# Kernel optimization log

Hardware: AMD Instinct MI355X
Metric: run time of the kernel (lower is better)

The kernel has to match this reference:

```python
import math
import jax, jax.numpy as jnp
import numpy as np

B, L, D, H, DFF = 2, 2048, 1024, 16, 4096
HD = D // H
NUM_BUCKETS, MAX_DISTANCE = 32, 128


def setup_inputs() -> dict:
    key = jax.random.key(0)
    ks = jax.random.split(key, 10)
    s = 0.02
    return {
        "hidden_states": jax.random.normal(ks[0], (B, L, D), dtype=jnp.float32),
        "Wq": jax.random.normal(ks[1], (D, D), dtype=jnp.float32) * s,
        "Wk": jax.random.normal(ks[2], (D, D), dtype=jnp.float32) * s,
        "Wv": jax.random.normal(ks[3], (D, D), dtype=jnp.float32) * s,
        "Wo": jax.random.normal(ks[4], (D, D), dtype=jnp.float32) * s,
        "W1": jax.random.normal(ks[5], (D, DFF), dtype=jnp.float32) * s,
        "W2": jax.random.normal(ks[6], (DFF, D), dtype=jnp.float32) * s,
        "ln1_g": jnp.ones((D,), dtype=jnp.float32),
        "ln2_g": jnp.ones((D,), dtype=jnp.float32),
        "rel_table": jax.random.normal(ks[7], (NUM_BUCKETS, H), dtype=jnp.float32) * s,
    }


def rms_norm(x, g, eps=1e-6):
    # T5-style LayerNorm: scale only, no mean subtraction
    var = jnp.mean(jnp.square(x.astype(jnp.float32)), axis=-1, keepdims=True)
    return (x.astype(jnp.float32) * jax.lax.rsqrt(var + eps)).astype(x.dtype) * g


def relative_position_bias(seq_len, table):
    # bidirectional T5 bucket scheme, num_buckets=32, max_distance=128
    ctx = jnp.arange(seq_len)[:, None]
    mem = jnp.arange(seq_len)[None, :]
    rp = mem - ctx                                  # (L, L) int
    nb = NUM_BUCKETS // 2
    buckets = (rp > 0).astype(jnp.int32) * nb
    rpa = jnp.abs(rp)
    max_exact = nb // 2
    is_small = rpa < max_exact
    safe = jnp.maximum(rpa, 1).astype(jnp.float32)  # avoid log(0); masked by is_small
    large = max_exact + (
        jnp.log(safe / max_exact) / math.log(MAX_DISTANCE / max_exact) * (nb - max_exact)
    ).astype(jnp.int32)
    large = jnp.minimum(large, nb - 1)
    buckets = buckets + jnp.where(is_small, rpa, large)   # (L, L)
    vals = table[buckets]                                  # (L, L, H)
    return jnp.transpose(vals, (2, 0, 1))[None]            # (1, H, L, L)


def reference(hidden_states, Wq, Wk, Wv, Wo, W1, W2, ln1_g, ln2_g, rel_table):
    x = hidden_states
    b, l, d = x.shape

    # --- self-attention sublayer (pre-norm) ---
    h = rms_norm(x, ln1_g)
    q = (h @ Wq).reshape(b, l, H, HD)
    k = (h @ Wk).reshape(b, l, H, HD)
    v = (h @ Wv).reshape(b, l, H, HD)

    bias = relative_position_bias(l, rel_table)            # (1, H, L, L)
    # NOTE: source's manual attention path has NO 1/sqrt(head_dim) scaling
    scores = jnp.einsum("bqhd,bkhd->bhqk", q, k) + bias
    attn = jax.nn.softmax(scores.astype(jnp.float32), axis=-1).astype(scores.dtype)
    out = jnp.einsum("bhqk,bkhd->bqhd", attn, v).reshape(b, l, d)
    x = x + out @ Wo

    # --- feed-forward sublayer (pre-norm) ---
    h = rms_norm(x, ln2_g)
    x = x + jax.nn.relu(h @ W1) @ W2
    return x
```

## Files before the change

kernel.cpp:

```cpp
#include <hip/hip_runtime.h>
#include <hip/hip_bf16.h>
#include <math.h>

#define BDIM 1024
#define HEADS 16
#define HDIM 64
#define LSEQ 2048
#define NBATCH 2
#define DFFDIM 4096
#define QKVN 3072
#define LOG2E 1.44269504f

typedef __bf16 bf16x8_t __attribute__((ext_vector_type(8)));
typedef float f32x4_t __attribute__((ext_vector_type(4)));

__device__ __forceinline__ ushort f2bf(float f) {
    union { __hip_bfloat16 b; ushort u; } cv;
    cv.b = __float2bfloat16(f);
    return cv.u;
}
__device__ __forceinline__ float bf2f(ushort u) {
    union { unsigned int i; float f; } cv;
    cv.i = ((unsigned int)u) << 16;
    return cv.f;
}

__global__ __launch_bounds__(256) void transpose_cvt(const float* __restrict__ W,
                                                     ushort* __restrict__ Wt,
                                                     int K, int N) {
    __shared__ ushort tile[32][33];
    int bi = blockIdx.y;
    int bj = blockIdx.x;
    int tx = threadIdx.x;
    int ty = threadIdx.y;
#pragma unroll
    for (int r = 0; r < 4; ++r) {
        int krow = bi * 32 + ty + r * 8;
        int ncol = bj * 32 + tx;
        tile[ty + r * 8][tx] = f2bf(W[(size_t)krow * N + ncol]);
    }
    __syncthreads();
#pragma unroll
    for (int r = 0; r < 4; ++r) {
        int nrow = bj * 32 + ty + r * 8;
        int kcol = bi * 32 + tx;
        Wt[(size_t)nrow * K + kcol] = tile[tx][ty + r * 8];
    }
}

__global__ __launch_bounds__(256) void vtrans(const ushort* __restrict__ qkv,
                                              ushort* __restrict__ vT) {
    __shared__ ushort t[64][72];
    const int ktile = blockIdx.x;
    const int bh = blockIdx.y;
    const int b = bh >> 4, h = bh & 15;
    const int tid = threadIdx.x;
    const int r = tid >> 2;
    const int c0 = (tid & 3) * 16;
    const ushort* src = qkv + (size_t)(b * LSEQ + ktile * 64 + r) * QKVN + 2048 + h * HDIM + c0;
    union { bf16x8_t v; ushort s[8]; } u0, u1;
    u0.v = *(const bf16x8_t*)src;
    u1.v = *(const bf16x8_t*)(src + 8);
#pragma unroll
    for (int j = 0; j < 8; ++j) { t[r][c0 + j] = u0.s[j]; t[r][c0 + 8 + j] = u1.s[j]; }
    __syncthreads();
    const int hd = tid >> 2;
    union { bf16x8_t v; ushort s[8]; } w0, w1;
#pragma unroll
    for (int j = 0; j < 8; ++j) { w0.s[j] = t[c0 + j][hd]; w1.s[j] = t[c0 + 8 + j][hd]; }
    ushort* dst = vT + (size_t)(bh * HDIM + hd) * LSEQ + ktile * 64 + c0;
    *(bf16x8_t*)dst = w0.v;
    *(bf16x8_t*)(dst + 8) = w1.v;
}

__global__ __launch_bounds__(256) void rmsnorm_k(const float* __restrict__ x,
                                                 const float* __restrict__ g,
                                                 ushort* __restrict__ out) {
    int row = blockIdx.x;
    int t = threadIdx.x;
    int w = t >> 6, l = t & 63;
    const float4 v = reinterpret_cast<const float4*>(x + (size_t)row * BDIM)[t];
    float ss = v.x * v.x + v.y * v.y + v.z * v.z + v.w * v.w;
#pragma unroll
    for (int m = 1; m <= 32; m <<= 1) ss += __shfl_xor(ss, m);
    __shared__ float wsum[4];
    if (l == 0) wsum[w] = ss;
    __syncthreads();
    float tot = wsum[0] + wsum[1] + wsum[2] + wsum[3];
    float r = rsqrtf(tot * (1.0f / BDIM) + 1e-6f);
    const float4 gv = reinterpret_cast<const float4*>(g)[t];
    ushort4 o;
    o.x = f2bf(v.x * r * gv.x);
    o.y = f2bf(v.y * r * gv.y);
    o.z = f2bf(v.z * r * gv.z);
    o.w = f2bf(v.w * r * gv.w);
    reinterpret_cast<ushort4*>(out + (size_t)row * BDIM)[t] = o;
}

__global__ void bias_table_k(const float* __restrict__ rel, float* __restrict__ btab) {
    int idx = blockIdx.x * 256 + threadIdx.x;
    if (idx >= HEADS * 4095) return;
    int h = idx / 4095;
    int d = idx % 4095;
    int rp = d - 2047;
    int bucket = rp > 0 ? 16 : 0;
    int rpa = rp < 0 ? -rp : rp;
    if (rpa < 8) {
        bucket += rpa;
    } else {
        int large = 8 + (int)(logf((float)rpa * 0.125f) * (1.0f / logf(16.0f)) * 8.0f);
        bucket += large < 15 ? large : 15;
    }
    btab[idx] = rel[bucket * HEADS + h];
}

__global__ __launch_bounds__(256) void reduce2_k(const ushort* __restrict__ parts,
                                                 const float* __restrict__ res,
                                                 float* __restrict__ out,
                                                 size_t mn) {
    size_t i = ((size_t)blockIdx.x * 256 + threadIdx.x) * 4;
    float4 r = *(const float4*)(res + i);
    ushort4 a = *(const ushort4*)(parts + i);
    ushort4 b = *(const ushort4*)(parts + mn + i);
    float4 o;
    o.x = r.x + bf2f(a.x) + bf2f(b.x);
    o.y = r.y + bf2f(a.y) + bf2f(b.y);
    o.z = r.z + bf2f(a.z) + bf2f(b.z);
    o.w = r.w + bf2f(a.w) + bf2f(b.w);
    *(float4*)(out + i) = o;
}

__global__ __launch_bounds__(256) void reduce2_rms(const ushort* __restrict__ parts,
                                                   const float* __restrict__ res,
                                                   const float* __restrict__ g,
                                                   float* __restrict__ out,
                                                   ushort* __restrict__ hout,
                                                   size_t mn) {
    int row = blockIdx.x;
    int t = threadIdx.x;
    int w = t >> 6, l = t & 63;
    size_t i = (size_t)row * BDIM + t * 4;
    float4 r = *(const float4*)(res + i);
    ushort4 a = *(const ushort4*)(parts + i);
    ushort4 b = *(const ushort4*)(parts + mn + i);
    float4 o;
    o.x = r.x + bf2f(a.x) + bf2f(b.x);
    o.y = r.y + bf2f(a.y) + bf2f(b.y);
    o.z = r.z + bf2f(a.z) + bf2f(b.z);
    o.w = r.w + bf2f(a.w) + bf2f(b.w);
    *(float4*)(out + i) = o;
    float ss = o.x * o.x + o.y * o.y + o.z * o.z + o.w * o.w;
#pragma unroll
    for (int m = 1; m <= 32; m <<= 1) ss += __shfl_xor(ss, m);
    __shared__ float wsum[4];
    if (l == 0) wsum[w] = ss;
    __syncthreads();
    float tot = wsum[0] + wsum[1] + wsum[2] + wsum[3];
    float rr = rsqrtf(tot * (1.0f / BDIM) + 1e-6f);
    const float4 gv = reinterpret_cast<const float4*>(g)[t];
    ushort4 h;
    h.x = f2bf(o.x * rr * gv.x);
    h.y = f2bf(o.y * rr * gv.y);
    h.z = f2bf(o.z * rr * gv.z);
    h.w = f2bf(o.w * rr * gv.w);
    reinterpret_cast<ushort4*>(hout + (size_t)row * BDIM)[t] = h;
}

template <int MODE, int TM, int TN>
__global__ __launch_bounds__(256) void gemm_bt(const ushort* __restrict__ A,
                                               const ushort* __restrict__ Bt,
                                               void* Cout, const float* res,
                                               int M, int N, int K, int nbx, int nkc) {
    __shared__ __align__(16) ushort As[TM * 64];
    __shared__ __align__(16) ushort Bs[TN * 64];
    constexpr int MF = TM / 32, NF = TN / 32;
    const int nwg = gridDim.x;
    const int bid = blockIdx.x;
    const int swz = (bid & 7) * (nwg >> 3) + (bid >> 3);
    const int nxy = nwg / nkc;
    const int chunk = swz / nxy;
    const int bxy = swz % nxy;
    const int bx = bxy % nbx, by = bxy / nbx;
    const int Kc = K / nkc;
    const int kbeg = chunk * Kc;
    const int tid = threadIdx.x;
    const int w = tid >> 6, l = tid & 63;
    const int wm = w >> 1, wn = w & 1;
    const int rowA0 = by * TM;
    const int colB0 = bx * TN;
    const int lr = l >> 3;
    const int scs = ((l & 7) ^ lr) * 8;
    const int c = l & 15, gq = l >> 4;
    const int rswz = (c & 7) * 8;
    f32x4_t acc[MF][NF] = {};

    auto stage = [&](int k0) {
#pragma unroll
        for (int i = 0; i < TM / 32; ++i) {
            int r = i * 32 + w * 8;
            __builtin_amdgcn_global_load_lds(
                (const __attribute__((address_space(1))) uint32_t*)(A + (size_t)(rowA0 + r + lr) * K + kbeg + k0 + scs),
                (__attribute__((address_space(3))) uint32_t*)(&As[r * 64]), 16, 0, 0);
        }
#pragma unroll
        for (int i = 0; i < TN / 32; ++i) {
            int r = i * 32 + w * 8;
            __builtin_amdgcn_global_load_lds(
                (const __attribute__((address_space(1))) uint32_t*)(Bt + (size_t)(colB0 + r + lr) * K + kbeg + k0 + scs),
                (__attribute__((address_space(3))) uint32_t*)(&Bs[r * 64]), 16, 0, 0);
        }
    };

    const int nk = Kc >> 6;
    for (int kt = 0; kt < nk; ++kt) {
        __syncthreads();
        stage(kt << 6);
        __syncthreads();
#pragma unroll
        for (int kk = 0; kk < 2; ++kk) {
            bf16x8_t av[MF], bv[NF];
#pragma unroll
            for (int mf = 0; mf < MF; ++mf)
                av[mf] = *(const bf16x8_t*)&As[(wm * (TM / 2) + mf * 16 + c) * 64 + ((kk * 32 + gq * 8) ^ rswz)];
#pragma unroll
            for (int nf = 0; nf < NF; ++nf)
                bv[nf] = *(const bf16x8_t*)&Bs[(wn * (TN / 2) + nf * 16 + c) * 64 + ((kk * 32 + gq * 8) ^ rswz)];
#pragma unroll
            for (int mf = 0; mf < MF; ++mf)
#pragma unroll
                for (int nf = 0; nf < NF; ++nf)
                    acc[mf][nf] = __builtin_amdgcn_mfma_f32_16x16x32_bf16(av[mf], bv[nf], acc[mf][nf], 0, 0, 0);
        }
    }
#pragma unroll
    for (int mf = 0; mf < MF; ++mf) {
#pragma unroll
        for (int nf = 0; nf < NF; ++nf) {
#pragma unroll
            for (int i = 0; i < 4; ++i) {
                int row = rowA0 + wm * (TM / 2) + mf * 16 + gq * 4 + i;
                int col = colB0 + wn * (TN / 2) + nf * 16 + c;
                size_t idx = (size_t)row * N + col;
                float vv = acc[mf][nf][i];
                if (MODE == 0) {
                    ((ushort*)Cout)[idx] = f2bf(vv);
                } else if (MODE == 1) {
                    ((float*)Cout)[idx] = res[idx] + vv;
                } else if (MODE == 2) {
                    ((ushort*)Cout)[idx] = f2bf(vv > 0.f ? vv : 0.f);
                } else {
                    ((ushort*)Cout)[(size_t)chunk * M * N + idx] = f2bf(vv);
                }
            }
        }
    }
}

__global__ __launch_bounds__(512) void attn_fwd(const ushort* __restrict__ qkv,
                                                const ushort* __restrict__ vT,
                                                const float* __restrict__ btab,
                                                ushort* __restrict__ ob) {
    const int tid = threadIdx.x, w = tid >> 6, l = tid & 63;
    const int bh = blockIdx.y, b = bh >> 4, h = bh & 15;
    const int qt = blockIdx.x;
    __shared__ __align__(16) ushort Ks[2][64 * 64];
    __shared__ __align__(16) ushort Vs[2][64 * 64];
    __shared__ __align__(16) ushort Pl[8][16 * 72];
    const int q0 = qt * 128 + w * 16;
    const int c = l & 15, g = l >> 4;
    const size_t rowbase = (size_t)b * LSEQ * QKVN;
    const ushort* qp = qkv + rowbase + h * HDIM;
    const ushort* kp = qkv + rowbase + BDIM + h * HDIM;
    const ushort* vtp = vT + (size_t)bh * HDIM * LSEQ;
    const int sr = tid >> 3;
    const int scs = ((l & 7) ^ (l >> 3)) * 8;
    const float* btq4 = btab + h * 4095 + 2047 - (q0 + c) + g * 4;

    bf16x8_t aq[2];
#pragma unroll
    for (int kk = 0; kk < 2; ++kk)
        aq[kk] = *(const bf16x8_t*)(qp + (size_t)(q0 + c) * QKVN + kk * 32 + g * 8);

    float mrow = -INFINITY, lrow = 0.f, m2 = -INFINITY;
    f32x4_t o[4] = {};
    f32x4_t s[4];

    auto stage = [&](int buf, int key0) {
        __builtin_amdgcn_global_load_lds(
            (const __attribute__((address_space(1))) uint32_t*)(kp + (size_t)(key0 + sr) * QKVN + scs),
            (__attribute__((address_space(3))) uint32_t*)(&Ks[buf][(w * 8) * 64]), 16, 0, 0);
        __builtin_amdgcn_global_load_lds(
            (const __attribute__((address_space(1))) uint32_t*)(vtp + (size_t)sr * LSEQ + key0 + scs),
            (__attribute__((address_space(3))) uint32_t*)(&Vs[buf][(w * 8) * 64]), 16, 0, 0);
    };
    auto loadBias = [&](int key0) {
#pragma unroll
        for (int nf = 0; nf < 4; ++nf)
#pragma unroll
            for (int i = 0; i < 4; ++i)
                s[nf][i] = btq4[key0 + nf * 16 + i];
    };

    stage(0, 0);
    loadBias(0);
    int cur = 0;

    ushort* Pw = Pl[w];
    const int rswz = (c & 7) << 3;
    for (int kt = 0; kt < 32; ++kt) {
        __syncthreads();
        if (kt < 31) stage(cur ^ 1, kt * 64 + 64);
        __builtin_amdgcn_s_setprio(1);
#pragma unroll
        for (int kk = 0; kk < 2; ++kk)
#pragma unroll
            for (int nf = 0; nf < 4; ++nf) {
                bf16x8_t kf = *(const bf16x8_t*)&Ks[cur][(nf * 16 + c) * 64 + ((kk * 32 + g * 8) ^ rswz)];
                s[nf] = __builtin_amdgcn_mfma_f32_16x16x32_bf16(kf, aq[kk], s[nf], 0, 0, 0);
            }
        __builtin_amdgcn_s_setprio(0);
        float tmax = fmaxf(
            fmaxf(fmaxf(fmaxf(s[0][0], s[0][1]), fmaxf(s[0][2], s[0][3])),
                  fmaxf(fmaxf(s[1][0], s[1][1]), fmaxf(s[1][2], s[1][3]))),
            fmaxf(fmaxf(fmaxf(s[2][0], s[2][1]), fmaxf(s[2][2], s[2][3])),
                  fmaxf(fmaxf(s[3][0], s[3][1]), fmaxf(s[3][2], s[3][3]))));
        tmax = fmaxf(tmax, __shfl_xor(tmax, 16));
        tmax = fmaxf(tmax, __shfl_xor(tmax, 32));
        if (!__all(tmax - mrow <= 8.f)) {
            float mn = fmaxf(mrow, tmax);
            float sc2 = exp2f((mrow - mn) * LOG2E);
            mrow = mn;
            m2 = mn * LOG2E;
            lrow *= sc2;
#pragma unroll
            for (int hf = 0; hf < 4; ++hf) o[hf] *= sc2;
        }
        float rs = 0.f;
        union { ushort us[4]; uint2 u2; } pk[4];
#pragma unroll
        for (int nf = 0; nf < 4; ++nf)
#pragma unroll
            for (int i = 0; i < 4; ++i) {
                float pv = exp2f(fmaf(s[nf][i], LOG2E, -m2));
                rs += pv;
                pk[nf].us[i] = f2bf(pv);
            }
        if (kt < 31) loadBias(kt * 64 + 64);
        rs += __shfl_xor(rs, 16);
        rs += __shfl_xor(rs, 32);
        lrow += rs;
#pragma unroll
        for (int nf = 0; nf < 4; ++nf)
            *(uint2*)&Pw[c * 72 + nf * 16 + g * 4] = pk[nf].u2;
        bf16x8_t pa[2];
#pragma unroll
        for (int kk = 0; kk < 2; ++kk)
            pa[kk] = *(const bf16x8_t*)&Pw[c * 72 + kk * 32 + g * 8];
        __builtin_amdgcn_s_setprio(1);
#pragma unroll
        for (int kk = 0; kk < 2; ++kk)
#pragma unroll
            for (int hf = 0; hf < 4; ++hf) {
                bf16x8_t vf = *(const bf16x8_t*)&Vs[cur][(hf * 16 + c) * 64 + ((kk * 32 + g * 8) ^ rswz)];
                o[hf] = __builtin_amdgcn_mfma_f32_16x16x32_bf16(vf, pa[kk], o[hf], 0, 0, 0);
            }
        __builtin_amdgcn_s_setprio(0);
        cur ^= 1;
    }
    const float inv = 1.f / lrow;
    ushort* orow = ob + (size_t)(b * LSEQ + q0 + c) * BDIM + h * HDIM + g * 4;
#pragma unroll
    for (int hf = 0; hf < 4; ++hf) {
        ushort4 ov;
        ov.x = f2bf(o[hf][0] * inv);
        ov.y = f2bf(o[hf][1] * inv);
        ov.z = f2bf(o[hf][2] * inv);
        ov.w = f2bf(o[hf][3] * inv);
        *(ushort4*)(orow + hf * 16) = ov;
    }
}

extern "C" void kernel_launch(void* const* d_in, const int* in_sizes, int n_in,
                              void* d_out, int out_size, void* d_ws, size_t ws_size,
                              hipStream_t stream) {
    const float* x   = (const float*)d_in[0];
    const float* Wq  = (const float*)d_in[1];
    const float* Wk  = (const float*)d_in[2];
    const float* Wv  = (const float*)d_in[3];
    const float* Wo  = (const float*)d_in[4];
    const float* W1  = (const float*)d_in[5];
    const float* W2  = (const float*)d_in[6];
    const float* g1  = (const float*)d_in[7];
    const float* g2  = (const float*)d_in[8];
    const float* rel = (const float*)d_in[9];
    float* out = (float*)d_out;

    char* ws = (char*)d_ws;
    const size_t MB = 1024 * 1024;
    ushort* wqkvT = (ushort*)(ws + 0 * MB);
    ushort* woT   = (ushort*)(ws + 6 * MB);
    ushort* w1T   = (ushort*)(ws + 8 * MB);
    ushort* w2T   = (ushort*)(ws + 16 * MB);
    float*  btab  = (float*)(ws + 24 * MB);
    ushort* hbuf  = (ushort*)(ws + 25 * MB);
    ushort* qkvb  = (ushort*)(ws + 33 * MB);
    ushort* woP   = (ushort*)(ws + 33 * MB);
    ushort* f1b   = (ushort*)(ws + 33 * MB);
    ushort* vTb   = (ushort*)(ws + 57 * MB);
    ushort* w2P   = (ushort*)(ws + 0 * MB);
    (void)in_sizes; (void)n_in; (void)out_size; (void)ws_size;

    const size_t MN = (size_t)4096 * 1024;
    dim3 tb(32, 8);
    transpose_cvt<<<dim3(32, 32),  tb, 0, stream>>>(Wq, wqkvT,                1024, 1024);
    transpose_cvt<<<dim3(32, 32),  tb, 0, stream>>>(Wk, wqkvT + 1024 * 1024,  1024, 1024);
    transpose_cvt<<<dim3(32, 32),  tb, 0, stream>>>(Wv, wqkvT + 2048 * 1024,  1024, 1024);
    transpose_cvt<<<dim3(32, 32),  tb, 0, stream>>>(Wo, woT, 1024, 1024);
    transpose_cvt<<<dim3(128, 32), tb, 0, stream>>>(W1, w1T, 1024, 4096);
    transpose_cvt<<<dim3(32, 128), tb, 0, stream>>>(W2, w2T, 4096, 1024);
    bias_table_k<<<256, 256, 0, stream>>>(rel, btab);

    rmsnorm_k<<<4096, 256, 0, stream>>>(x, g1, hbuf);
    gemm_bt<0, 128, 128><<<768, 256, 0, stream>>>(hbuf, wqkvT, qkvb, nullptr, 4096, QKVN, 1024, 24, 1);
    vtrans<<<dim3(32, 32), 256, 0, stream>>>(qkvb, vTb);
    attn_fwd<<<dim3(16, 32), 512, 0, stream>>>(qkvb, vTb, btab, hbuf);
    gemm_bt<3, 128, 128><<<512, 256, 0, stream>>>(hbuf, woT, woP, nullptr, 4096, 1024, 1024, 8, 2);
    reduce2_rms<<<4096, 256, 0, stream>>>(woP, x, g2, out, hbuf, MN);
    gemm_bt<2, 128, 128><<<1024, 256, 0, stream>>>(hbuf, w1T, f1b, nullptr, 4096, DFFDIM, 1024, 32, 1);
    gemm_bt<3, 128, 128><<<512, 256, 0, stream>>>(f1b, w2T, w2P, nullptr, 4096, 1024, 4096, 8, 2);
    reduce2_k<<<4096, 256, 0, stream>>>(w2P, out, out, MN);
}
```

Baseline: 259.6 us.

## Triple-buffer attention K/V tiles, stage bias in LDS, retile output GEMMs

The attention kernel moves from double to triple-buffered K/V staging, waiting on explicit vmcnt counts and a raw s_barrier so two tiles stay in flight. The per-block slice of the relative-position bias row is copied into shared memory once, so the per-tile bias loads no longer go to global memory. It also drops the setprio hints and switches exp2f with a log2e multiply to __expf. Separately, the Wo and W2 split-K GEMMs use 128x64 tiles with twice as many blocks, trading more blocks for less work per block. LDS use per block rises, which may lower occupancy.

Result: no change. 256.9 us (-1.0%).

```diff
diff --git a/kernel.cpp b/kernel.cpp
--- a/kernel.cpp
+++ b/kernel.cpp
@@ -9,7 +9,6 @@
 #define NBATCH 2
 #define DFFDIM 4096
 #define QKVN 3072
-#define LOG2E 1.44269504f
 
 typedef __bf16 bf16x8_t __attribute__((ext_vector_type(8)));
 typedef float f32x4_t __attribute__((ext_vector_type(4)));
@@ -263,10 +262,12 @@
     const int tid = threadIdx.x, w = tid >> 6, l = tid & 63;
     const int bh = blockIdx.y, b = bh >> 4, h = bh & 15;
     const int qt = blockIdx.x;
-    __shared__ __align__(16) ushort Ks[2][64 * 64];
-    __shared__ __align__(16) ushort Vs[2][64 * 64];
+    __shared__ __align__(16) ushort Ks[3][64 * 64];
+    __shared__ __align__(16) ushort Vs[3][64 * 64];
     __shared__ __align__(16) ushort Pl[8][16 * 72];
-    const int q0 = qt * 128 + w * 16;
+    __shared__ float Bl[2176];
+    const int Q0 = qt * 128;
+    const int q0 = Q0 + w * 16;
     const int c = l & 15, g = l >> 4;
     const size_t rowbase = (size_t)b * LSEQ * QKVN;
     const ushort* qp = qkv + rowbase + h * HDIM;
@@ -274,14 +275,17 @@
     const ushort* vtp = vT + (size_t)bh * HDIM * LSEQ;
     const int sr = tid >> 3;
     const int scs = ((l & 7) ^ (l >> 3)) * 8;
-    const float* btq4 = btab + h * 4095 + 2047 - (q0 + c) + g * 4;
+
+    const float* btabh = btab + h * 4095 + 1920 - Q0;
+    for (int t = tid; t < 2175; t += 512) Bl[t] = btabh[t];
+    const float* bl = Bl + 127 + g * 4 - (w * 16 + c);
 
     bf16x8_t aq[2];
 #pragma unroll
     for (int kk = 0; kk < 2; ++kk)
         aq[kk] = *(const bf16x8_t*)(qp + (size_t)(q0 + c) * QKVN + kk * 32 + g * 8);
 
-    float mrow = -INFINITY, lrow = 0.f, m2 = -INFINITY;
+    float mrow = -INFINITY, lrow = 0.f;
     f32x4_t o[4] = {};
     f32x4_t s[4];
 
@@ -298,19 +302,23 @@
         for (int nf = 0; nf < 4; ++nf)
 #pragma unroll
             for (int i = 0; i < 4; ++i)
-                s[nf][i] = btq4[key0 + nf * 16 + i];
+                s[nf][i] = bl[key0 + nf * 16 + i];
     };
 
+    __syncthreads();
     stage(0, 0);
+    stage(1, 64);
     loadBias(0);
-    int cur = 0;
 
     ushort* Pw = Pl[w];
     const int rswz = (c & 7) << 3;
     for (int kt = 0; kt < 32; ++kt) {
-        __syncthreads();
-        if (kt < 31) stage(cur ^ 1, kt * 64 + 64);
-        __builtin_amdgcn_s_setprio(1);
+        if (kt < 31) asm volatile("s_waitcnt vmcnt(2)" ::: "memory");
+        else         asm volatile("s_waitcnt vmcnt(0)" ::: "memory");
+        __builtin_amdgcn_s_barrier();
+        __builtin_amdgcn_sched_barrier(0);
+        if (kt < 30) stage((kt + 2) % 3, (kt + 2) * 64);
+        const int cur = kt % 3;
 #pragma unroll
         for (int kk = 0; kk < 2; ++kk)
 #pragma unroll
@@ -318,19 +326,18 @@
                 bf16x8_t kf = *(const bf16x8_t*)&Ks[cur][(nf * 16 + c) * 64 + ((kk * 32 + g * 8) ^ rswz)];
                 s[nf] = __builtin_amdgcn_mfma_f32_16x16x32_bf16(kf, aq[kk], s[nf], 0, 0, 0);
             }
-        __builtin_amdgcn_s_setprio(0);
-        float tmax = fmaxf(
-            fmaxf(fmaxf(fmaxf(s[0][0], s[0][1]), fmaxf(s[0][2], s[0][3])),
-                  fmaxf(fmaxf(s[1][0], s[1][1]), fmaxf(s[1][2], s[1][3]))),
-            fmaxf(fmaxf(fmaxf(s[2][0], s[2][1]), fmaxf(s[2][2], s[2][3])),
-                  fmaxf(fmaxf(s[3][0], s[3][1]), fmaxf(s[3][2], s[3][3]))));
+        float tmax = -INFINITY;
+#pragma unroll
+        for (int nf = 0; nf < 4; ++nf)
+#pragma unroll
+            for (int i = 0; i < 4; ++i)
+                tmax = fmaxf(tmax, s[nf][i]);
         tmax = fmaxf(tmax, __shfl_xor(tmax, 16));
         tmax = fmaxf(tmax, __shfl_xor(tmax, 32));
         if (!__all(tmax - mrow <= 8.f)) {
             float mn = fmaxf(mrow, tmax);
-            float sc2 = exp2f((mrow - mn) * LOG2E);
+            float sc2 = __expf(mrow - mn);
             mrow = mn;
-            m2 = mn * LOG2E;
             lrow *= sc2;
 #pragma unroll
             for (int hf = 0; hf < 4; ++hf) o[hf] *= sc2;
@@ -341,7 +348,7 @@
         for (int nf = 0; nf < 4; ++nf)
 #pragma unroll
             for (int i = 0; i < 4; ++i) {
-                float pv = exp2f(fmaf(s[nf][i], LOG2E, -m2));
+                float pv = __expf(s[nf][i] - mrow);
                 rs += pv;
                 pk[nf].us[i] = f2bf(pv);
             }
@@ -356,7 +363,6 @@
 #pragma unroll
         for (int kk = 0; kk < 2; ++kk)
             pa[kk] = *(const bf16x8_t*)&Pw[c * 72 + kk * 32 + g * 8];
-        __builtin_amdgcn_s_setprio(1);
 #pragma unroll
         for (int kk = 0; kk < 2; ++kk)
 #pragma unroll
@@ -364,8 +370,6 @@
                 bf16x8_t vf = *(const bf16x8_t*)&Vs[cur][(hf * 16 + c) * 64 + ((kk * 32 + g * 8) ^ rswz)];
                 o[hf] = __builtin_amdgcn_mfma_f32_16x16x32_bf16(vf, pa[kk], o[hf], 0, 0, 0);
             }
-        __builtin_amdgcn_s_setprio(0);
-        cur ^= 1;
     }
     const float inv = 1.f / lrow;
     ushort* orow = ob + (size_t)(b * LSEQ + q0 + c) * BDIM + h * HDIM + g * 4;
@@ -424,9 +428,9 @@
     gemm_bt<0, 128, 128><<<768, 256, 0, stream>>>(hbuf, wqkvT, qkvb, nullptr, 4096, QKVN, 1024, 24, 1);
     vtrans<<<dim3(32, 32), 256, 0, stream>>>(qkvb, vTb);
     attn_fwd<<<dim3(16, 32), 512, 0, stream>>>(qkvb, vTb, btab, hbuf);
-    gemm_bt<3, 128, 128><<<512, 256, 0, stream>>>(hbuf, woT, woP, nullptr, 4096, 1024, 1024, 8, 2);
+    gemm_bt<3, 128, 64><<<1024, 256, 0, stream>>>(hbuf, woT, woP, nullptr, 4096, 1024, 1024, 16, 2);
     reduce2_rms<<<4096, 256, 0, stream>>>(woP, x, g2, out, hbuf, MN);
     gemm_bt<2, 128, 128><<<1024, 256, 0, stream>>>(hbuf, w1T, f1b, nullptr, 4096, DFFDIM, 1024, 32, 1);
-    gemm_bt<3, 128, 128><<<512, 256, 0, stream>>>(f1b, w2T, w2P, nullptr, 4096, 1024, 4096, 8, 2);
+    gemm_bt<3, 128, 64><<<1024, 256, 0, stream>>>(f1b, w2T, w2P, nullptr, 4096, 1024, 4096, 16, 2);
     reduce2_k<<<4096, 256, 0, stream>>>(w2P, out, out, MN);
 }
```
